# Performance work log

Hardware: AMD Instinct MI355X
Metric: run time of the kernel (lower is better)

Reference implementation:

```python
import jax, jax.numpy as jnp
import numpy as np

N, C, H, W, G = 8, 256, 128, 128, 32
STRIDE = 8


def setup_inputs() -> dict:
    key = jax.random.key(0)
    kx, kxy, kwh = jax.random.split(key, 3)
    x = jax.random.normal(kx, (N, C, H, W), dtype=jnp.float32)
    # valid pixel-space boxes: x1,y1 in [0, 900), w,h in [16, 200)
    xy1 = jax.random.uniform(kxy, (N, G, 2), minval=0.0, maxval=900.0)
    wh = jax.random.uniform(kwh, (N, G, 2), minval=16.0, maxval=200.0)
    xy2 = jnp.clip(xy1 + wh, 0.0, STRIDE * W - 1.0)
    gt_bboxes = jnp.concatenate([xy1, xy2], axis=-1).astype(jnp.float32)  # [N,G,4] (x1,y1,x2,y2)
    return {"x": x, "gt_bboxes": gt_bboxes, "stride": STRIDE, "epoch": 5}


def reference(x, gt_bboxes, stride, epoch):
    # x: [N,C,H,W]; gt_bboxes: [N,G,4] pixel coords (x1,y1,x2,y2)
    n, c, h, w = x.shape
    b = gt_bboxes / stride
    x1 = jnp.floor(b[..., 0])  # [N,G]
    y1 = jnp.floor(b[..., 1])
    x2 = jnp.ceil(b[..., 2])
    y2 = jnp.ceil(b[..., 3])
    ys = jnp.arange(h, dtype=b.dtype)
    xs = jnp.arange(w, dtype=b.dtype)
    # inside tests, vectorized over all boxes (replaces per-bbox slice assignment)
    in_y = (ys[None, None, :] >= y1[..., None]) & (ys[None, None, :] < y2[..., None])  # [N,G,H]
    in_x = (xs[None, None, :] >= x1[..., None]) & (xs[None, None, :] < x2[..., None])  # [N,G,W]
    mask = jnp.any(in_y[:, :, :, None] & in_x[:, :, None, :], axis=1)  # [N,H,W], union of boxes
    mask = mask.astype(x.dtype)
    # channel-mean of masked (detached) features, scaled by cosine schedule
    e = jnp.mean(jax.lax.stop_gradient(x) * mask[:, None, :, :], axis=1, keepdims=True)  # [N,1,H,W]
    alpha = 0.5 * (1.0 + jnp.cos(jnp.pi * epoch / 22.0))
    excitations = jax.lax.stop_gradient(e * alpha)
    return x + excitations  # broadcast over channel dim
```

## Files before the change

kernel.cpp:

```cpp
#include <hip/hip_runtime.h>
#include <math.h>

constexpr int N_ = 8, C_ = 256, H_ = 128, W_ = 128, G_ = 32;
constexpr int HW  = H_ * W_;
constexpr int CHW = C_ * HW;
constexpr int TPIX = 64;

typedef float f4 __attribute__((ext_vector_type(4)));

__global__ __launch_bounds__(512) void fused_exc_kernel(
    const float* __restrict__ x, const float* __restrict__ bb,
    const int* __restrict__ stride_p, const int* __restrict__ epoch_p,
    float* __restrict__ out)
{
    __shared__ f4 psum[8][16];

    int bid  = blockIdx.x;
    int n    = bid >> 8;
    int rem  = bid & 255;
    int row  = rem >> 1;
    int half = rem & 1;

    int tid  = threadIdx.x;
    int wv   = tid >> 6;
    int lane = tid & 63;
    int c0   = tid >> 4;
    int q    = tid & 15;

    size_t goff = (size_t)n * CHW + (size_t)c0 * HW + (size_t)row * W_ + half * TPIX + q * 4;
    const float* xp = x + goff;

    f4 v[8];
    #pragma unroll
    for (int k = 0; k < 8; ++k)
        v[k] = *reinterpret_cast<const f4*>(xp + (size_t)(32 * k) * HW);

    float inv   = 1.0f / (float)(*stride_p);
    float alpha = 0.5f * (1.0f + cosf((float)M_PI * (float)(*epoch_p) / 22.0f));
    float scale = alpha / (float)C_;

    float hf = (float)row;
    float w0 = (float)(half * TPIX + q * 4);
    const f4* bbp = reinterpret_cast<const f4*>(bb) + n * G_;
    int m = 0;
    #pragma unroll 4
    for (int g = 0; g < G_; ++g) {
        f4 bv = bbp[g];
        float x1 = floorf(bv.x * inv), y1 = floorf(bv.y * inv);
        float x2 = ceilf (bv.z * inv), y2 = ceilf (bv.w * inv);
        if (hf >= y1 && hf < y2) {
            #pragma unroll
            for (int j = 0; j < 4; ++j) {
                float wf = w0 + (float)j;
                if (wf >= x1 && wf < x2) m |= 1 << j;
            }
        }
    }

    f4 s = v[0];
    #pragma unroll
    for (int k = 1; k < 8; ++k) s += v[k];
    s.x += __shfl_xor(s.x, 16); s.y += __shfl_xor(s.y, 16);
    s.z += __shfl_xor(s.z, 16); s.w += __shfl_xor(s.w, 16);
    s.x += __shfl_xor(s.x, 32); s.y += __shfl_xor(s.y, 32);
    s.z += __shfl_xor(s.z, 32); s.w += __shfl_xor(s.w, 32);
    if (lane < 16) psum[wv][q] = s;
    __syncthreads();

    f4 sum = psum[0][q];
    #pragma unroll
    for (int w = 1; w < 8; ++w) sum += psum[w][q];

    f4 e4;
    e4.x = (m & 1) ? sum.x * scale : 0.f;
    e4.y = (m & 2) ? sum.y * scale : 0.f;
    e4.z = (m & 4) ? sum.z * scale : 0.f;
    e4.w = (m & 8) ? sum.w * scale : 0.f;

    float* op = out + goff;
    #pragma unroll
    for (int k = 0; k < 8; ++k) {
        f4 o = v[k] + e4;
        __builtin_nontemporal_store(o, reinterpret_cast<f4*>(op + (size_t)(32 * k) * HW));
    }
}

extern "C" void kernel_launch(void* const* d_in, const int* in_sizes, int n_in,
                              void* d_out, int out_size, void* d_ws, size_t ws_size,
                              hipStream_t stream) {
    const float* x  = (const float*)d_in[0];
    const float* bb = (const float*)d_in[1];
    const int* stride_p = (const int*)d_in[2];
    const int* epoch_p  = (const int*)d_in[3];
    float* out = (float*)d_out;

    int grid = N_ * H_ * 2;
    fused_exc_kernel<<<grid, 512, 0, stream>>>(x, bb, stride_p, epoch_p, out);
}
```

Baseline: 47.72 us.

## Map one wavefront per 16-pixel strip to drop shared-memory reduction and barrier

Each wavefront now owns 16 consecutive pixels across all 256 channels, with every lane loading 16 channels of four pixels, so the channel sum is finished entirely with wave shuffles. The shared-memory partial sums and the block barrier go away, and blocks shrink to 256 threads. The cost is more live registers per thread (16 float4 values) and only 64-byte contiguous segments per channel row, which may lower memory coalescing efficiency.

```diff
diff --git a/kernel.cpp b/kernel.cpp
--- a/kernel.cpp
+++ b/kernel.cpp
@@ -4,43 +4,38 @@
 constexpr int N_ = 8, C_ = 256, H_ = 128, W_ = 128, G_ = 32;
 constexpr int HW  = H_ * W_;
 constexpr int CHW = C_ * HW;
-constexpr int TPIX = 64;
 
 typedef float f4 __attribute__((ext_vector_type(4)));
 
-__global__ __launch_bounds__(512) void fused_exc_kernel(
+__global__ __launch_bounds__(256, 4) void fused_exc_kernel(
     const float* __restrict__ x, const float* __restrict__ bb,
     const int* __restrict__ stride_p, const int* __restrict__ epoch_p,
     float* __restrict__ out)
 {
-    __shared__ f4 psum[8][16];
+    int tid   = blockIdx.x * 256 + threadIdx.x;
+    int lane  = tid & 63;
+    int gw    = tid >> 6;
+    int chunk = lane >> 2;
+    int q     = lane & 3;
 
-    int bid  = blockIdx.x;
-    int n    = bid >> 8;
-    int rem  = bid & 255;
-    int row  = rem >> 1;
-    int half = rem & 1;
+    int pix0 = gw << 4;
+    int n    = pix0 >> 14;
+    int hw   = pix0 & (HW - 1);
 
-    int tid  = threadIdx.x;
-    int wv   = tid >> 6;
-    int lane = tid & 63;
-    int c0   = tid >> 4;
-    int q    = tid & 15;
-
-    size_t goff = (size_t)n * CHW + (size_t)c0 * HW + (size_t)row * W_ + half * TPIX + q * 4;
+    size_t goff = (size_t)n * CHW + (size_t)(chunk * 16) * HW + (size_t)hw + q * 4;
     const float* xp = x + goff;
 
-    f4 v[8];
+    f4 v[16];
     #pragma unroll
-    for (int k = 0; k < 8; ++k)
-        v[k] = *reinterpret_cast<const f4*>(xp + (size_t)(32 * k) * HW);
+    for (int k = 0; k < 16; ++k)
+        v[k] = *reinterpret_cast<const f4*>(xp + (size_t)k * HW);
 
     float inv   = 1.0f / (float)(*stride_p);
     float alpha = 0.5f * (1.0f + cosf((float)M_PI * (float)(*epoch_p) / 22.0f));
     float scale = alpha / (float)C_;
 
-    float hf = (float)row;
-    float w0 = (float)(half * TPIX + q * 4);
+    float hf = (float)(hw >> 7);
+    float w0 = (float)((hw & 127) + q * 4);
     const f4* bbp = reinterpret_cast<const f4*>(bb) + n * G_;
     int m = 0;
     #pragma unroll 4
@@ -59,29 +54,27 @@
 
     f4 s = v[0];
     #pragma unroll
-    for (int k = 1; k < 8; ++k) s += v[k];
-    s.x += __shfl_xor(s.x, 16); s.y += __shfl_xor(s.y, 16);
-    s.z += __shfl_xor(s.z, 16); s.w += __shfl_xor(s.w, 16);
-    s.x += __shfl_xor(s.x, 32); s.y += __shfl_xor(s.y, 32);
-    s.z += __shfl_xor(s.z, 32); s.w += __shfl_xor(s.w, 32);
-    if (lane < 16) psum[wv][q] = s;
-    __syncthreads();
+    for (int k = 1; k < 16; ++k) s += v[k];
 
-    f4 sum = psum[0][q];
     #pragma unroll
-    for (int w = 1; w < 8; ++w) sum += psum[w][q];
+    for (int off = 4; off <= 32; off <<= 1) {
+        s.x += __shfl_xor(s.x, off);
+        s.y += __shfl_xor(s.y, off);
+        s.z += __shfl_xor(s.z, off);
+        s.w += __shfl_xor(s.w, off);
+    }
 
     f4 e4;
-    e4.x = (m & 1) ? sum.x * scale : 0.f;
-    e4.y = (m & 2) ? sum.y * scale : 0.f;
-    e4.z = (m & 4) ? sum.z * scale : 0.f;
-    e4.w = (m & 8) ? sum.w * scale : 0.f;
+    e4.x = (m & 1) ? s.x * scale : 0.f;
+    e4.y = (m & 2) ? s.y * scale : 0.f;
+    e4.z = (m & 4) ? s.z * scale : 0.f;
+    e4.w = (m & 8) ? s.w * scale : 0.f;
 
     float* op = out + goff;
     #pragma unroll
-    for (int k = 0; k < 8; ++k) {
+    for (int k = 0; k < 16; ++k) {
         f4 o = v[k] + e4;
-        __builtin_nontemporal_store(o, reinterpret_cast<f4*>(op + (size_t)(32 * k) * HW));
+        __builtin_nontemporal_store(o, reinterpret_cast<f4*>(op + (size_t)k * HW));
     }
 }
 
@@ -94,6 +87,6 @@
     const int* epoch_p  = (const int*)d_in[3];
     float* out = (float*)d_out;
 
-    int grid = N_ * H_ * 2;
-    fused_exc_kernel<<<grid, 512, 0, stream>>>(x, bb, stride_p, epoch_p, out);
+    int grid = (N_ * HW / 16) / 4;
+    fused_exc_kernel<<<grid, 256, 0, stream>>>(x, bb, stride_p, epoch_p, out);
 }
```

Measured after the change: 56.73 us. 1.19x slower.

## Process four tiles per block with software-pipelined loads and double-buffered reductions

Applied to the files above, without the earlier changes.

Each block now handles two rows and both halves of each row, four tiles in all, so the grid shrinks to a quarter of its former size. Loads for later tiles are issued before the reduction and store of earlier tiles. Two shared buffers take turns holding the partial sums, and a lighter barrier (lgkmcnt wait plus s_barrier) replaces __syncthreads. The goal is to overlap memory latency with the reduction barrier and to compute box masks for four tiles in one loop. The cost is much higher register pressure (four register arrays of 8 f4 each) and fewer blocks for a kernel that is already close to bandwidth-bound.

```diff
diff --git a/kernel.cpp b/kernel.cpp
--- a/kernel.cpp
+++ b/kernel.cpp
@@ -4,22 +4,65 @@
 constexpr int N_ = 8, C_ = 256, H_ = 128, W_ = 128, G_ = 32;
 constexpr int HW  = H_ * W_;
 constexpr int CHW = C_ * HW;
-constexpr int TPIX = 64;
 
 typedef float f4 __attribute__((ext_vector_type(4)));
+
+__device__ __forceinline__ void softbar() {
+    asm volatile("s_waitcnt lgkmcnt(0)\n\ts_barrier" ::: "memory");
+}
+
+__device__ __forceinline__ f4 wave_reduce(const f4* v) {
+    f4 s = v[0];
+    #pragma unroll
+    for (int k = 1; k < 8; ++k) s += v[k];
+    s.x += __shfl_xor(s.x, 16); s.y += __shfl_xor(s.y, 16);
+    s.z += __shfl_xor(s.z, 16); s.w += __shfl_xor(s.w, 16);
+    s.x += __shfl_xor(s.x, 32); s.y += __shfl_xor(s.y, 32);
+    s.z += __shfl_xor(s.z, 32); s.w += __shfl_xor(s.w, 32);
+    return s;
+}
+
+__device__ __forceinline__ f4 block_sum(const f4 (*buf)[16], int q) {
+    f4 sum = buf[0][q];
+    #pragma unroll
+    for (int w = 1; w < 8; ++w) sum += buf[w][q];
+    return sum;
+}
+
+__device__ __forceinline__ f4 make_e(int m, f4 sum, float scale) {
+    f4 e;
+    e.x = (m & 1) ? sum.x * scale : 0.f;
+    e.y = (m & 2) ? sum.y * scale : 0.f;
+    e.z = (m & 4) ? sum.z * scale : 0.f;
+    e.w = (m & 8) ? sum.w * scale : 0.f;
+    return e;
+}
+
+__device__ __forceinline__ void load_tile(f4* v, const float* xp) {
+    #pragma unroll
+    for (int k = 0; k < 8; ++k)
+        v[k] = *reinterpret_cast<const f4*>(xp + (size_t)(32 * k) * HW);
+}
+
+__device__ __forceinline__ void store_tile(float* op, const f4* v, f4 e) {
+    #pragma unroll
+    for (int k = 0; k < 8; ++k) {
+        f4 o = v[k] + e;
+        __builtin_nontemporal_store(o, reinterpret_cast<f4*>(op + (size_t)(32 * k) * HW));
+    }
+}
 
 __global__ __launch_bounds__(512) void fused_exc_kernel(
     const float* __restrict__ x, const float* __restrict__ bb,
     const int* __restrict__ stride_p, const int* __restrict__ epoch_p,
     float* __restrict__ out)
 {
-    __shared__ f4 psum[8][16];
+    __shared__ f4 psum[2][8][16];
 
     int bid  = blockIdx.x;
-    int n    = bid >> 8;
-    int rem  = bid & 255;
-    int row  = rem >> 1;
-    int half = rem & 1;
+    int n    = bid >> 6;
+    int rp   = bid & 63;
+    int row0 = rp << 1;
 
     int tid  = threadIdx.x;
     int wv   = tid >> 6;
@@ -27,62 +70,54 @@
     int c0   = tid >> 4;
     int q    = tid & 15;
 
-    size_t goff = (size_t)n * CHW + (size_t)c0 * HW + (size_t)row * W_ + half * TPIX + q * 4;
-    const float* xp = x + goff;
+    size_t base = (size_t)n * CHW + (size_t)c0 * HW + (size_t)row0 * W_ + q * 4;
+    size_t g0 = base, g1 = base + 64, g2 = base + W_, g3 = base + W_ + 64;
 
-    f4 v[8];
-    #pragma unroll
-    for (int k = 0; k < 8; ++k)
-        v[k] = *reinterpret_cast<const f4*>(xp + (size_t)(32 * k) * HW);
+    f4 v0[8], v1[8], v2[8], v3[8];
+    load_tile(v0, x + g0);
+    load_tile(v1, x + g1);
 
     float inv   = 1.0f / (float)(*stride_p);
     float alpha = 0.5f * (1.0f + cosf((float)M_PI * (float)(*epoch_p) / 22.0f));
     float scale = alpha / (float)C_;
 
-    float hf = (float)row;
-    float w0 = (float)(half * TPIX + q * 4);
+    float hf0 = (float)row0, hf1 = (float)(row0 + 1);
+    float wA  = (float)(q * 4), wB = wA + 64.0f;
     const f4* bbp = reinterpret_cast<const f4*>(bb) + n * G_;
-    int m = 0;
+    int m0 = 0, m1 = 0, m2 = 0, m3 = 0;
     #pragma unroll 4
     for (int g = 0; g < G_; ++g) {
         f4 bv = bbp[g];
-        float x1 = floorf(bv.x * inv), y1 = floorf(bv.y * inv);
-        float x2 = ceilf (bv.z * inv), y2 = ceilf (bv.w * inv);
-        if (hf >= y1 && hf < y2) {
-            #pragma unroll
-            for (int j = 0; j < 4; ++j) {
-                float wf = w0 + (float)j;
-                if (wf >= x1 && wf < x2) m |= 1 << j;
-            }
+        float bx1 = floorf(bv.x * inv), by1 = floorf(bv.y * inv);
+        float bx2 = ceilf (bv.z * inv), by2 = ceilf (bv.w * inv);
+        int wa = 0, wb = 0;
+        #pragma unroll
+        for (int j = 0; j < 4; ++j) {
+            float fA = wA + (float)j, fB = wB + (float)j;
+            if (fA >= bx1 && fA < bx2) wa |= 1 << j;
+            if (fB >= bx1 && fB < bx2) wb |= 1 << j;
         }
+        if (hf0 >= by1 && hf0 < by2) { m0 |= wa; m1 |= wb; }
+        if (hf1 >= by1 && hf1 < by2) { m2 |= wa; m3 |= wb; }
     }
 
-    f4 s = v[0];
-    #pragma unroll
-    for (int k = 1; k < 8; ++k) s += v[k];
-    s.x += __shfl_xor(s.x, 16); s.y += __shfl_xor(s.y, 16);
-    s.z += __shfl_xor(s.z, 16); s.w += __shfl_xor(s.w, 16);
-    s.x += __shfl_xor(s.x, 32); s.y += __shfl_xor(s.y, 32);
-    s.z += __shfl_xor(s.z, 32); s.w += __shfl_xor(s.w, 32);
-    if (lane < 16) psum[wv][q] = s;
-    __syncthreads();
+    { f4 s = wave_reduce(v0); if (lane < 16) psum[0][wv][q] = s; }
+    load_tile(v2, x + g2);
+    softbar();
+    store_tile(out + g0, v0, make_e(m0, block_sum(psum[0], q), scale));
 
-    f4 sum = psum[0][q];
-    #pragma unroll
-    for (int w = 1; w < 8; ++w) sum += psum[w][q];
+    { f4 s = wave_reduce(v1); if (lane < 16) psum[1][wv][q] = s; }
+    load_tile(v3, x + g3);
+    softbar();
+    store_tile(out + g1, v1, make_e(m1, block_sum(psum[1], q), scale));
 
-    f4 e4;
-    e4.x = (m & 1) ? sum.x * scale : 0.f;
-    e4.y = (m & 2) ? sum.y * scale : 0.f;
-    e4.z = (m & 4) ? sum.z * scale : 0.f;
-    e4.w = (m & 8) ? sum.w * scale : 0.f;
+    { f4 s = wave_reduce(v2); if (lane < 16) psum[0][wv][q] = s; }
+    softbar();
+    store_tile(out + g2, v2, make_e(m2, block_sum(psum[0], q), scale));
 
-    float* op = out + goff;
-    #pragma unroll
-    for (int k = 0; k < 8; ++k) {
-        f4 o = v[k] + e4;
-        __builtin_nontemporal_store(o, reinterpret_cast<f4*>(op + (size_t)(32 * k) * HW));
-    }
+    { f4 s = wave_reduce(v3); if (lane < 16) psum[1][wv][q] = s; }
+    softbar();
+    store_tile(out + g3, v3, make_e(m3, block_sum(psum[1], q), scale));
 }
 
 extern "C" void kernel_launch(void* const* d_in, const int* in_sizes, int n_in,
@@ -94,6 +129,6 @@
     const int* epoch_p  = (const int*)d_in[3];
     float* out = (float*)d_out;
 
-    int grid = N_ * H_ * 2;
+    int grid = N_ * H_ / 2;
     fused_exc_kernel<<<grid, 512, 0, stream>>>(x, bb, stride_p, epoch_p, out);
 }
```

Result: slower. 53.51 us (+12.1%).
